# Kernel optimization log

Measured on AMD Instinct MI355X. Metric: run time of the kernel, lower is better.

## Reference

```python
import jax, jax.numpy as jnp
import numpy as np

HIDDEN = 1024
NUM_HEADS = 16
HEAD_DIM = HIDDEN // NUM_HEADS  # 64
B, S = 4, 1024


def setup_inputs() -> dict:
    key = jax.random.key(0)
    ks = jax.random.split(key, 8)
    xavier = jax.nn.initializers.xavier_uniform()
    inputs = jax.random.normal(ks[0], (B, S, HIDDEN), dtype=jnp.float32)
    context = jax.random.normal(ks[1], (B, S, HIDDEN), dtype=jnp.float32)
    # multiplicative mask: 1 = attend, 0 = ignore (causal), broadcast over batch/heads
    mask = jnp.tril(jnp.ones((S, S), dtype=jnp.float32))[None, None, :, :]
    Wq = xavier(ks[2], (HIDDEN, HIDDEN), jnp.float32)
    bq = jnp.zeros((HIDDEN,), jnp.float32)
    Wk = xavier(ks[3], (HIDDEN, HEAD_DIM), jnp.float32)
    bk = jnp.zeros((HEAD_DIM,), jnp.float32)
    Wv = xavier(ks[4], (HIDDEN, HEAD_DIM), jnp.float32)
    bv = jnp.zeros((HEAD_DIM,), jnp.float32)
    Wo = xavier(ks[5], (HIDDEN, HIDDEN), jnp.float32)
    bo = jnp.zeros((HIDDEN,), jnp.float32)
    return {"inputs": inputs, "context": context, "mask": mask,
            "Wq": Wq, "bq": bq, "Wk": Wk, "bk": bk,
            "Wv": Wv, "bv": bv, "Wo": Wo, "bo": bo}


def reference(inputs, context, mask, Wq, bq, Wk, bk, Wv, bv, Wo, bo):
    query = inputs @ Wq + bq                      # (B, S, D)
    key = context @ Wk + bk                       # (B, S, D/H)
    value = context @ Wv + bv                     # (B, S, D/H)
    # MQA: broadcast single KV head to all query heads via interleaved repeat
    key = jnp.repeat(key, NUM_HEADS, axis=-1)     # (B, S, D)
    value = jnp.repeat(value, NUM_HEADS, axis=-1) # (B, S, D)
    bsz = query.shape[0]
    Lq, Lk = query.shape[1], key.shape[1]
    # faithful to original: plain reshape (not transpose) into heads
    qh = jnp.reshape(query, (bsz, NUM_HEADS, Lq, HEAD_DIM))
    kh = jnp.reshape(key, (bsz, NUM_HEADS, Lk, HEAD_DIM))
    vh = jnp.reshape(value, (bsz, NUM_HEADS, Lk, HEAD_DIM))
    # note: original scales by sqrt(key.shape[-1]) == sqrt(hidden_dim)
    scores = jnp.einsum('bhqd,bhkd->bhqk', qh, kh) / jnp.sqrt(jnp.float32(HIDDEN))
    scores = scores * mask                        # multiplicative mask
    attn = jax.nn.softmax(scores, axis=-1)        # (B, H, Lq, Lk)
    ctx = jnp.einsum('bhqk,bhkd->bhqd', attn, vh)
    ctx = jnp.reshape(ctx, (bsz, Lq, HIDDEN))
    outputs = ctx @ Wo + bo                       # (B, S, D)
    return outputs, attn
```

## Files before the change

kernel.cpp:

```cpp
#include <hip/hip_runtime.h>
#include <hip/hip_bf16.h>
#include <cstdint>

#define NHEADS 16
#define SEQ    1024
#define BATCH  4

typedef float vfloat4 __attribute__((ext_vector_type(4)));

__device__ __forceinline__ float wave_sum(float v){
  #pragma unroll
  for (int off = 32; off > 0; off >>= 1) v += __shfl_xor(v, off);
  return v;
}
__device__ __forceinline__ void nt_store4(float* p, float x, float y, float z, float w){
  vfloat4 v; v.x = x; v.y = y; v.z = z; v.w = w;
  __builtin_nontemporal_store(v, (vfloat4*)p);
}

__global__ __launch_bounds__(256) void prep_kernel(
    const float* __restrict__ Wq, const float* __restrict__ bq,
    const float* __restrict__ Wo,
    float* __restrict__ WqSum, float* __restrict__ bqSum, float* __restrict__ WoSum)
{
  const int blk = blockIdx.x, tid = threadIdx.x;
  if (blk < 256){
    const int c = blk * 4 + (tid >> 6), g = tid & 63;
    const float* p = &Wq[(size_t)c * 1024 + (g << 4)];
    float s = 0.f;
    #pragma unroll
    for (int f = 0; f < 16; ++f) s += p[f];
    WqSum[c * 64 + g] = s;
  } else if (blk < 320){
    const int g = blk - 256;
    for (int m = tid; m < 1024; m += 256){
      float s = 0.f;
      #pragma unroll
      for (int f = 0; f < 16; ++f) s += Wo[(size_t)((g << 4) + f) * 1024 + m];
      WoSum[g * 1024 + m] = s;
    }
  } else {
    if (tid < 64){
      float s = 0.f;
      #pragma unroll
      for (int f = 0; f < 16; ++f) s += bq[(tid << 4) + f];
      bqSum[tid] = s;
    }
  }
}

__global__ __launch_bounds__(256) void qkv_split(
    const float* __restrict__ inputs, const float* __restrict__ context,
    const float* __restrict__ WqSum,
    const float* __restrict__ Wk, const float* __restrict__ Wv,
    float* __restrict__ part)
{
  __shared__ float As[2][16][68];
  __shared__ float Bs[2][16][68];
  const int z = blockIdx.y, sz = blockIdx.z;
  const float* A = (z == 0) ? inputs : context;
  const float* B = (z == 0) ? WqSum : ((z == 1) ? Wk : Wv);
  const int m0 = blockIdx.x * 64;
  const int ks = sz << 8;
  const int tid = threadIdx.x;
  const int tx = tid & 15, ty = tid >> 4;
  const int arow = tid >> 2, acg = (tid & 3) << 2;
  const int brow = tid >> 4, bcg = (tid & 15) << 2;

  float4 av  = *(const float4*)&A[(size_t)(m0 + arow) * 1024 + ks + acg];
  float4 bvv = *(const float4*)&B[(size_t)(ks + brow) * 64 + bcg];
  As[0][acg + 0][arow] = av.x; As[0][acg + 1][arow] = av.y;
  As[0][acg + 2][arow] = av.z; As[0][acg + 3][arow] = av.w;
  *(float4*)&Bs[0][brow][bcg] = bvv;
  __syncthreads();

  float acc[4][4] = {};
  for (int t = 0; t < 16; ++t){
    const int cur = t & 1;
    if (t < 15){
      const int k0 = ks + ((t + 1) << 4);
      av  = *(const float4*)&A[(size_t)(m0 + arow) * 1024 + k0 + acg];
      bvv = *(const float4*)&B[(size_t)(k0 + brow) * 64 + bcg];
    }
    #pragma unroll
    for (int kk = 0; kk < 16; ++kk){
      const float4 a  = *(const float4*)&As[cur][kk][ty << 2];
      const float4 bb = *(const float4*)&Bs[cur][kk][tx << 2];
      const float a_[4] = {a.x, a.y, a.z, a.w};
      const float b_[4] = {bb.x, bb.y, bb.z, bb.w};
      #pragma unroll
      for (int i = 0; i < 4; ++i)
        #pragma unroll
        for (int j = 0; j < 4; ++j) acc[i][j] += a_[i] * b_[j];
    }
    if (t < 15){
      As[cur ^ 1][acg + 0][arow] = av.x; As[cur ^ 1][acg + 1][arow] = av.y;
      As[cur ^ 1][acg + 2][arow] = av.z; As[cur ^ 1][acg + 3][arow] = av.w;
      *(float4*)&Bs[cur ^ 1][brow][bcg] = bvv;
    }
    __syncthreads();
  }
  float* P = part + ((size_t)(z * 4 + sz) * 4096 + m0) * 64;
  #pragma unroll
  for (int i = 0; i < 4; ++i)
    *(float4*)&P[(size_t)((ty << 2) + i) * 64 + (tx << 2)] =
      make_float4(acc[i][0], acc[i][1], acc[i][2], acc[i][3]);
}

#define DOT_ROW(aq, q, t, MASKED) do {                                        \
  t.x = (aq.x*b0.x + aq.y*b1.x + aq.z*b2.x + aq.w*b3.x) * 0.03125f;           \
  t.y = (aq.x*b0.y + aq.y*b1.y + aq.z*b2.y + aq.w*b3.y) * 0.03125f;           \
  t.z = (aq.x*b0.z + aq.y*b1.z + aq.z*b2.z + aq.w*b3.z) * 0.03125f;           \
  t.w = (aq.x*b0.w + aq.y*b1.w + aq.z*b2.w + aq.w*b3.w) * 0.03125f;           \
  if (MASKED){                                                                \
    t.x = (k0     <= q) ? t.x : 0.0f;                                         \
    t.y = (k0 + 1 <= q) ? t.y : 0.0f;                                         \
    t.z = (k0 + 2 <= q) ? t.z : 0.0f;                                         \
    t.w = (k0 + 3 <= q) ? t.w : 0.0f;                                         \
  }                                                                           \
} while (0)

__global__ __launch_bounds__(256, 4) void attn_kernel(
    const float* __restrict__ part,
    const float* __restrict__ bqSum, const float* __restrict__ bk,
    const float* __restrict__ bv,
    float* __restrict__ Ctx, float* __restrict__ attnp)
{
  __shared__ float BmT[4][1032];
  __shared__ float VmT[4][1032];
  __shared__ float Aq[64][4];
  __shared__ float bsum16[16];
  __shared__ float SufT[4][5];

  const int tid = threadIdx.x;
  const int qb = (blockIdx.x + (blockIdx.z << 2)) & 15;
  const int h  = blockIdx.y;
  const int b  = blockIdx.z;
  const int base = b * SEQ + h * 64;

  for (int idx = tid; idx < 4096; idx += 256){
    const int r = idx >> 6, c = idx & 63;
    const size_t off = (size_t)(base + r) * 64 + c;
    float kacc = bk[c], vacc = bv[c];
    #pragma unroll
    for (int s = 0; s < 4; ++s){
      kacc += part[(size_t)(4 + s) * 262144 + off];
      vacc += part[(size_t)(8 + s) * 262144 + off];
    }
    const int k = (r << 4) + (c >> 2), e = c & 3;
    BmT[e][k] = kacc;
    VmT[e][k] = vacc;
  }
  {
    const int p_l = tid >> 6, g = tid & 63;
    float qacc = bqSum[g];
    const size_t off = (size_t)(base + (qb << 2) + p_l) * 64 + g;
    #pragma unroll
    for (int s = 0; s < 4; ++s) qacc += part[(size_t)s * 262144 + off];
    Aq[(p_l << 4) + (g >> 2)][g & 3] = qacc;
  }
  __syncthreads();
  {
    const int pair = tid >> 4, sub = tid & 15;
    const int e = pair >> 2, jj = pair & 3;
    float s = 0.f;
    #pragma unroll
    for (int n = 0; n < 16; ++n) s += VmT[e][(jj << 8) + (n << 4) + sub];
    #pragma unroll
    for (int off2 = 8; off2 > 0; off2 >>= 1) s += __shfl_xor(s, off2);
    if (sub == 0) bsum16[pair] = s;
  }
  __syncthreads();
  if (tid < 4){
    float s = 0.f;
    SufT[tid][4] = 0.f;
    for (int jj = 3; jj >= 0; --jj){ s += bsum16[tid * 4 + jj]; SufT[tid][jj] = s; }
  }
  __syncthreads();

  const int wave = tid >> 6, lane = tid & 63;
  const int jdot  = (qb >> 2) + 1;
  const int ktail = jdot << 8;
  const float ztail = (float)(1024 - ktail);
  const float suf0 = SufT[0][jdot], suf1 = SufT[1][jdot];
  const float suf2 = SufT[2][jdot], suf3 = SufT[3][jdot];

  for (int i = 0; i < 16; i += 4){
    const int qlA = (wave << 4) + i;
    const int qA  = (qb << 6) + qlA;
    const int qB = qA + 1, qC = qA + 2, qD = qA + 3;
    const float4 aA = *(const float4*)&Aq[qlA][0];
    const float4 aB = *(const float4*)&Aq[qlA + 1][0];
    const float4 aC = *(const float4*)&Aq[qlA + 2][0];
    const float4 aD = *(const float4*)&Aq[qlA + 3][0];
    float ZA = 0.f, ZB = 0.f, ZC = 0.f, ZD = 0.f;
    float cA0=0.f,cA1=0.f,cA2=0.f,cA3=0.f, cB0=0.f,cB1=0.f,cB2=0.f,cB3=0.f;
    float cC0=0.f,cC1=0.f,cC2=0.f,cC3=0.f, cD0=0.f,cD1=0.f,cD2=0.f,cD3=0.f;

    for (int j = 0; j < jdot; ++j){
      const int k0 = (lane << 2) + (j << 8);
      const float4 b0 = *(const float4*)&BmT[0][k0];
      const float4 b1 = *(const float4*)&BmT[1][k0];
      const float4 b2 = *(const float4*)&BmT[2][k0];
      const float4 b3 = *(const float4*)&BmT[3][k0];
      const float4 v0 = *(const float4*)&VmT[0][k0];
      const float4 v1 = *(const float4*)&VmT[1][k0];
      const float4 v2 = *(const float4*)&VmT[2][k0];
      const float4 v3 = *(const float4*)&VmT[3][k0];
      const bool bm = (j == jdot - 1);
      float4 t;
      DOT_ROW(aA, qA, t, bm);
      {
        const float e0 = __expf(t.x), e1 = __expf(t.y);
        const float e2 = __expf(t.z), e3 = __expf(t.w);
        ZA += (e0 + e1) + (e2 + e3);
        cA0 += e0*v0.x + e1*v0.y + e2*v0.z + e3*v0.w;
        cA1 += e0*v1.x + e1*v1.y + e2*v1.z + e3*v1.w;
        cA2 += e0*v2.x + e1*v2.y + e2*v2.z + e3*v2.w;
        cA3 += e0*v3.x + e1*v3.y + e2*v3.z + e3*v3.w;
      }
      DOT_ROW(aB, qB, t, bm);
      {
        const float e0 = __expf(t.x), e1 = __expf(t.y);
        const float e2 = __expf(t.z), e3 = __expf(t.w);
        ZB += (e0 + e1) + (e2 + e3);
        cB0 += e0*v0.x + e1*v0.y + e2*v0.z + e3*v0.w;
        cB1 += e0*v1.x + e1*v1.y + e2*v1.z + e3*v1.w;
        cB2 += e0*v2.x + e1*v2.y + e2*v2.z + e3*v2.w;
        cB3 += e0*v3.x + e1*v3.y + e2*v3.z + e3*v3.w;
      }
      DOT_ROW(aC, qC, t, bm);
      {
        const float e0 = __expf(t.x), e1 = __expf(t.y);
        const float e2 = __expf(t.z), e3 = __expf(t.w);
        ZC += (e0 + e1) + (e2 + e3);
        cC0 += e0*v0.x + e1*v0.y + e2*v0.z + e3*v0.w;
        cC1 += e0*v1.x + e1*v1.y + e2*v1.z + e3*v1.w;
        cC2 += e0*v2.x + e1*v2.y + e2*v2.z + e3*v2.w;
        cC3 += e0*v3.x + e1*v3.y + e2*v3.z + e3*v3.w;
      }
      DOT_ROW(aD, qD, t, bm);
      {
        const float e0 = __expf(t.x), e1 = __expf(t.y);
        const float e2 = __expf(t.z), e3 = __expf(t.w);
        ZD += (e0 + e1) + (e2 + e3);
        cD0 += e0*v0.x + e1*v0.y + e2*v0.z + e3*v0.w;
        cD1 += e0*v1.x + e1*v1.y + e2*v1.z + e3*v1.w;
        cD2 += e0*v2.x + e1*v2.y + e2*v2.z + e3*v2.w;
        cD3 += e0*v3.x + e1*v3.y + e2*v3.z + e3*v3.w;
      }
    }
    const float ZAt = wave_sum(ZA) + ztail;
    const float ZBt = wave_sum(ZB) + ztail;
    const float ZCt = wave_sum(ZC) + ztail;
    const float ZDt = wave_sum(ZD) + ztail;
    cA0 = wave_sum(cA0) + suf0; cA1 = wave_sum(cA1) + suf1;
    cA2 = wave_sum(cA2) + suf2; cA3 = wave_sum(cA3) + suf3;
    cB0 = wave_sum(cB0) + suf0; cB1 = wave_sum(cB1) + suf1;
    cB2 = wave_sum(cB2) + suf2; cB3 = wave_sum(cB3) + suf3;
    cC0 = wave_sum(cC0) + suf0; cC1 = wave_sum(cC1) + suf1;
    cC2 = wave_sum(cC2) + suf2; cC3 = wave_sum(cC3) + suf3;
    cD0 = wave_sum(cD0) + suf0; cD1 = wave_sum(cD1) + suf1;
    cD2 = wave_sum(cD2) + suf2; cD3 = wave_sum(cD3) + suf3;
    const float invZA = 1.0f / ZAt, invZB = 1.0f / ZBt;
    const float invZC = 1.0f / ZCt, invZD = 1.0f / ZDt;

    float* rowA = attnp + (((size_t)(b * NHEADS + h) << 10) + (size_t)qA) * 1024;
    float* rowB = rowA + 1024;
    float* rowC = rowA + 2048;
    float* rowD = rowA + 3072;

    for (int j = 0; j < jdot; ++j){
      const int k0 = (lane << 2) + (j << 8);
      const float4 b0 = *(const float4*)&BmT[0][k0];
      const float4 b1 = *(const float4*)&BmT[1][k0];
      const float4 b2 = *(const float4*)&BmT[2][k0];
      const float4 b3 = *(const float4*)&BmT[3][k0];
      const bool bm = (j == jdot - 1);
      float4 t;
      DOT_ROW(aA, qA, t, bm);
      nt_store4(rowA + k0, __expf(t.x) * invZA, __expf(t.y) * invZA,
                           __expf(t.z) * invZA, __expf(t.w) * invZA);
      DOT_ROW(aB, qB, t, bm);
      nt_store4(rowB + k0, __expf(t.x) * invZB, __expf(t.y) * invZB,
                           __expf(t.z) * invZB, __expf(t.w) * invZB);
      DOT_ROW(aC, qC, t, bm);
      nt_store4(rowC + k0, __expf(t.x) * invZC, __expf(t.y) * invZC,
                           __expf(t.z) * invZC, __expf(t.w) * invZC);
      DOT_ROW(aD, qD, t, bm);
      nt_store4(rowD + k0, __expf(t.x) * invZD, __expf(t.y) * invZD,
                           __expf(t.z) * invZD, __expf(t.w) * invZD);
    }
    for (int rr = 0; rr < 4 - jdot; ++rr){
      const int kf = ktail + (rr << 8) + (lane << 2);
      nt_store4(rowA + kf, invZA, invZA, invZA, invZA);
      nt_store4(rowB + kf, invZB, invZB, invZB, invZB);
      nt_store4(rowC + kf, invZC, invZC, invZC, invZC);
      nt_store4(rowD + kf, invZD, invZD, invZD, invZD);
    }
    if (lane == 0){
      *(float4*)&Ctx[(size_t)(base + (qA >> 4)) * 64 + ((qA & 15) << 2)] =
        make_float4(cA0 * invZA, cA1 * invZA, cA2 * invZA, cA3 * invZA);
      *(float4*)&Ctx[(size_t)(base + (qB >> 4)) * 64 + ((qB & 15) << 2)] =
        make_float4(cB0 * invZB, cB1 * invZB, cB2 * invZB, cB3 * invZB);
      *(float4*)&Ctx[(size_t)(base + (qC >> 4)) * 64 + ((qC & 15) << 2)] =
        make_float4(cC0 * invZC, cC1 * invZC, cC2 * invZC, cC3 * invZC);
      *(float4*)&Ctx[(size_t)(base + (qD >> 4)) * 64 + ((qD & 15) << 2)] =
        make_float4(cD0 * invZD, cD1 * invZD, cD2 * invZD, cD3 * invZD);
    }
  }
}

__global__ __launch_bounds__(256) void out_gemm(
    const float* __restrict__ Ctx, const float* __restrict__ WoSum,
    const float* __restrict__ bo, float* __restrict__ outp)
{
  __shared__ float Cs[64][68];
  __shared__ float Ws[64][128];
  const int tid = threadIdx.x;
  const int m0 = blockIdx.x * 64, n0 = blockIdx.y * 128;

  for (int t = tid; t < 1024; t += 256){
    const int row = t >> 4, c4 = (t & 15) << 2;
    const float4 v = *(const float4*)&Ctx[(size_t)(m0 + row) * 64 + c4];
    Cs[c4 + 0][row] = v.x; Cs[c4 + 1][row] = v.y;
    Cs[c4 + 2][row] = v.z; Cs[c4 + 3][row] = v.w;
  }
  for (int t = tid; t < 2048; t += 256){
    const int row = t >> 5, c4 = (t & 31) << 2;
    *(float4*)&Ws[row][c4] = *(const float4*)&WoSum[(size_t)row * 1024 + n0 + c4];
  }
  __syncthreads();

  const int tx = tid & 31, ty = tid >> 5;
  float acc[8][4] = {};
  for (int kk = 0; kk < 64; ++kk){
    const float4 bb = *(const float4*)&Ws[kk][tx << 2];
    const float4 a0 = *(const float4*)&Cs[kk][ty << 3];
    const float4 a1 = *(const float4*)&Cs[kk][(ty << 3) + 4];
    const float a_[8] = {a0.x, a0.y, a0.z, a0.w, a1.x, a1.y, a1.z, a1.w};
    const float b_[4] = {bb.x, bb.y, bb.z, bb.w};
    #pragma unroll
    for (int i = 0; i < 8; ++i)
      #pragma unroll
      for (int j = 0; j < 4; ++j) acc[i][j] += a_[i] * b_[j];
  }
  const float4 bov = *(const float4*)&bo[n0 + (tx << 2)];
  #pragma unroll
  for (int i = 0; i < 8; ++i){
    nt_store4(&outp[(size_t)(m0 + (ty << 3) + i) * 1024 + n0 + (tx << 2)],
              acc[i][0] + bov.x, acc[i][1] + bov.y,
              acc[i][2] + bov.z, acc[i][3] + bov.w);
  }
}

extern "C" void kernel_launch(void* const* d_in, const int* in_sizes, int n_in,
                              void* d_out, int out_size, void* d_ws, size_t ws_size,
                              hipStream_t stream)
{
  const float* inputs  = (const float*)d_in[0];
  const float* context = (const float*)d_in[1];
  const float* Wq = (const float*)d_in[3];
  const float* bq = (const float*)d_in[4];
  const float* Wk = (const float*)d_in[5];
  const float* bk = (const float*)d_in[6];
  const float* Wv = (const float*)d_in[7];
  const float* bv = (const float*)d_in[8];
  const float* Wo = (const float*)d_in[9];
  const float* bo = (const float*)d_in[10];

  float* outp  = (float*)d_out;
  float* attnp = outp + (size_t)BATCH * SEQ * 1024;

  float* ws    = (float*)d_ws;
  float* WqSum = ws;
  float* bqSum = ws + 65536;
  float* WoSum = ws + 65600;
  float* Ctx   = ws + 131136;
  float* part  = ws + 393280;

  prep_kernel<<<dim3(321), dim3(256), 0, stream>>>(Wq, bq, Wo, WqSum, bqSum, WoSum);
  qkv_split <<<dim3(64, 3, 4), dim3(256), 0, stream>>>(inputs, context, WqSum,
                                                       Wk, Wv, part);
  attn_kernel<<<dim3(16, 16, 4), dim3(256), 0, stream>>>(part, bqSum, bk, bv,
                                                         Ctx, attnp);
  out_gemm  <<<dim3(64, 8), dim3(256), 0, stream>>>(Ctx, WoSum, bo, outp);
}
```

Measured before the change: 112.9 us.

## Split attention into normalizer/PV kernel and separate probability-render kernel

The attention kernel is split in two. The first computes the softmax normalizers and the context vectors, and saves the per-row query values and inverse normalizers to workspace. A second kernel rebuilds the key tile, recomputes the scores and streams the normalized attention probabilities out. This separates the register-heavy reduction phase from the store-bound output phase, which could improve occupancy and store throughput, at the cost of an extra launch and reloading K.

```diff
diff --git a/kernel.cpp b/kernel.cpp
--- a/kernel.cpp
+++ b/kernel.cpp
@@ -120,11 +120,11 @@
   }                                                                           \
 } while (0)
 
-__global__ __launch_bounds__(256, 4) void attn_kernel(
+__global__ __launch_bounds__(256, 4) void attn_zpv(
     const float* __restrict__ part,
     const float* __restrict__ bqSum, const float* __restrict__ bk,
     const float* __restrict__ bv,
-    float* __restrict__ Ctx, float* __restrict__ attnp)
+    float* __restrict__ Ctx, float* __restrict__ AqT, float* __restrict__ invZt)
 {
   __shared__ float BmT[4][1032];
   __shared__ float VmT[4][1032];
@@ -137,6 +137,7 @@
   const int h  = blockIdx.y;
   const int b  = blockIdx.z;
   const int base = b * SEQ + h * 64;
+  const size_t rowbase = ((size_t)(b * NHEADS + h) << 10) + (qb << 6);
 
   for (int idx = tid; idx < 4096; idx += 256){
     const int r = idx >> 6, c = idx & 63;
@@ -157,7 +158,9 @@
     const size_t off = (size_t)(base + (qb << 2) + p_l) * 64 + g;
     #pragma unroll
     for (int s = 0; s < 4; ++s) qacc += part[(size_t)s * 262144 + off];
-    Aq[(p_l << 4) + (g >> 2)][g & 3] = qacc;
+    const int ql = (p_l << 4) + (g >> 2);
+    Aq[ql][g & 3] = qacc;
+    AqT[(rowbase + ql) * 4 + (g & 3)] = qacc;
   }
   __syncthreads();
   {
@@ -265,39 +268,6 @@
     const float invZA = 1.0f / ZAt, invZB = 1.0f / ZBt;
     const float invZC = 1.0f / ZCt, invZD = 1.0f / ZDt;
 
-    float* rowA = attnp + (((size_t)(b * NHEADS + h) << 10) + (size_t)qA) * 1024;
-    float* rowB = rowA + 1024;
-    float* rowC = rowA + 2048;
-    float* rowD = rowA + 3072;
-
-    for (int j = 0; j < jdot; ++j){
-      const int k0 = (lane << 2) + (j << 8);
-      const float4 b0 = *(const float4*)&BmT[0][k0];
-      const float4 b1 = *(const float4*)&BmT[1][k0];
-      const float4 b2 = *(const float4*)&BmT[2][k0];
-      const float4 b3 = *(const float4*)&BmT[3][k0];
-      const bool bm = (j == jdot - 1);
-      float4 t;
-      DOT_ROW(aA, qA, t, bm);
-      nt_store4(rowA + k0, __expf(t.x) * invZA, __expf(t.y) * invZA,
-                           __expf(t.z) * invZA, __expf(t.w) * invZA);
-      DOT_ROW(aB, qB, t, bm);
-      nt_store4(rowB + k0, __expf(t.x) * invZB, __expf(t.y) * invZB,
-                           __expf(t.z) * invZB, __expf(t.w) * invZB);
-      DOT_ROW(aC, qC, t, bm);
-      nt_store4(rowC + k0, __expf(t.x) * invZC, __expf(t.y) * invZC,
-                           __expf(t.z) * invZC, __expf(t.w) * invZC);
-      DOT_ROW(aD, qD, t, bm);
-      nt_store4(rowD + k0, __expf(t.x) * invZD, __expf(t.y) * invZD,
-                           __expf(t.z) * invZD, __expf(t.w) * invZD);
-    }
-    for (int rr = 0; rr < 4 - jdot; ++rr){
-      const int kf = ktail + (rr << 8) + (lane << 2);
-      nt_store4(rowA + kf, invZA, invZA, invZA, invZA);
-      nt_store4(rowB + kf, invZB, invZB, invZB, invZB);
-      nt_store4(rowC + kf, invZC, invZC, invZC, invZC);
-      nt_store4(rowD + kf, invZD, invZD, invZD, invZD);
-    }
     if (lane == 0){
       *(float4*)&Ctx[(size_t)(base + (qA >> 4)) * 64 + ((qA & 15) << 2)] =
         make_float4(cA0 * invZA, cA1 * invZA, cA2 * invZA, cA3 * invZA);
@@ -307,6 +277,60 @@
         make_float4(cC0 * invZC, cC1 * invZC, cC2 * invZC, cC3 * invZC);
       *(float4*)&Ctx[(size_t)(base + (qD >> 4)) * 64 + ((qD & 15) << 2)] =
         make_float4(cD0 * invZD, cD1 * invZD, cD2 * invZD, cD3 * invZD);
+      *(float4*)&invZt[rowbase + qlA] =
+        make_float4(invZA, invZB, invZC, invZD);
+    }
+  }
+}
+
+__global__ __launch_bounds__(256) void attn_render(
+    const float* __restrict__ part, const float* __restrict__ bk,
+    const float* __restrict__ AqT, const float* __restrict__ invZt,
+    float* __restrict__ attnp)
+{
+  __shared__ float BmT[4][1032];
+
+  const int tid = threadIdx.x;
+  const int qb = (blockIdx.x + (blockIdx.z << 2)) & 15;
+  const int h  = blockIdx.y;
+  const int b  = blockIdx.z;
+  const int base = b * SEQ + h * 64;
+  const size_t rowbase = ((size_t)(b * NHEADS + h) << 10) + (qb << 6);
+
+  for (int idx = tid; idx < 4096; idx += 256){
+    const int r = idx >> 6, c = idx & 63;
+    const size_t off = (size_t)(base + r) * 64 + c;
+    float kacc = bk[c];
+    #pragma unroll
+    for (int s = 0; s < 4; ++s) kacc += part[(size_t)(4 + s) * 262144 + off];
+    BmT[c & 3][(r << 4) + (c >> 2)] = kacc;
+  }
+  __syncthreads();
+
+  const int wave = tid >> 6, lane = tid & 63;
+  const int jdot  = (qb >> 2) + 1;
+  const int ktail = jdot << 8;
+
+  for (int i = 0; i < 16; ++i){
+    const int ql = (wave << 4) + i;
+    const int q  = (qb << 6) + ql;
+    const float4 a  = *(const float4*)&AqT[(rowbase + ql) * 4];
+    const float invZ = invZt[rowbase + ql];
+    float* rowp = attnp + (rowbase + ql) * 1024;
+    for (int j = 0; j < jdot; ++j){
+      const int k0 = (lane << 2) + (j << 8);
+      const float4 b0 = *(const float4*)&BmT[0][k0];
+      const float4 b1 = *(const float4*)&BmT[1][k0];
+      const float4 b2 = *(const float4*)&BmT[2][k0];
+      const float4 b3 = *(const float4*)&BmT[3][k0];
+      const bool bm = (j == jdot - 1);
+      float4 t;
+      DOT_ROW(a, q, t, bm);
+      nt_store4(rowp + k0, __expf(t.x) * invZ, __expf(t.y) * invZ,
+                           __expf(t.z) * invZ, __expf(t.w) * invZ);
+    }
+    for (int rr = 0; rr < 4 - jdot; ++rr){
+      nt_store4(rowp + ktail + (rr << 8) + (lane << 2), invZ, invZ, invZ, invZ);
     }
   }
 }
@@ -377,12 +401,15 @@
   float* bqSum = ws + 65536;
   float* WoSum = ws + 65600;
   float* Ctx   = ws + 131136;
-  float* part  = ws + 393280;
+  float* AqT   = ws + 393280;
+  float* invZt = ws + 655424;
+  float* part  = ws + 720960;
 
   prep_kernel<<<dim3(321), dim3(256), 0, stream>>>(Wq, bq, Wo, WqSum, bqSum, WoSum);
-  qkv_split <<<dim3(64, 3, 4), dim3(256), 0, stream>>>(inputs, context, WqSum,
-                                                       Wk, Wv, part);
-  attn_kernel<<<dim3(16, 16, 4), dim3(256), 0, stream>>>(part, bqSum, bk, bv,
-                                                         Ctx, attnp);
-  out_gemm  <<<dim3(64, 8), dim3(256), 0, stream>>>(Ctx, WoSum, bo, outp);
-}
+  qkv_split  <<<dim3(64, 3, 4), dim3(256), 0, stream>>>(inputs, context, WqSum,
+                                                        Wk, Wv, part);
+  attn_zpv   <<<dim3(16, 16, 4), dim3(256), 0, stream>>>(part, bqSum, bk, bv,
+                                                         Ctx, AqT, invZt);
+  attn_render<<<dim3(16, 16, 4), dim3(256), 0, stream>>>(part, bk, AqT, invZt, attnp);
+  out_gemm   <<<dim3(64, 8), dim3(256), 0, stream>>>(Ctx, WoSum, bo, outp);
+}
```

Measured after the change: 155.3 us. 37.6% more time.
